# Optimization experiments

Hardware: AMD Instinct MI355X
Metric: run time of the kernel (lower is better)

## Reference

```python
import jax, jax.numpy as jnp
import numpy as np

B, TQ, TS, E, D = 8, 100, 100, 512, 512

def setup_inputs() -> dict:
    key = jax.random.key(0)
    k1, k2, k3, k4, k5 = jax.random.split(key, 5)
    src_reps = jax.random.normal(k1, (B, TQ, TS, E), dtype=jnp.float32)
    tgt_reps = jax.random.normal(k2, (B, TQ, TS, E), dtype=jnp.float32)
    mask = jnp.ones((B, TQ, TS), dtype=jnp.float32)
    # attn_1: Linear(2E -> D) with bias; attn_2: Linear(D -> 1) no bias
    W1 = jax.random.normal(k3, (2 * E, D), dtype=jnp.float32) / np.sqrt(2 * E)
    b1 = jax.random.normal(k4, (D,), dtype=jnp.float32) * 0.01
    w2 = jax.random.normal(k5, (D,), dtype=jnp.float32) / np.sqrt(D)
    return {"src_reps": src_reps, "tgt_reps": tgt_reps, "mask": mask,
            "W1": W1, "b1": b1, "w2": w2}

def reference(src_reps, tgt_reps, mask, W1, b1, w2):
    # cat over feature dim: [B,TQ,TS,2E]
    cat_reps = jnp.concatenate([src_reps, tgt_reps], axis=-1)
    # two small linears + tanh -> scores [B,TQ,TS]
    h = jnp.tanh(jnp.einsum('bqse,ed->bqsd', cat_reps, W1) + b1)
    attn_scores = jnp.einsum('bqsd,d->bqs', h, w2)
    attn_scores = mask * attn_scores  # multiplicative mask (as in source)
    attn_weights = jax.nn.softmax(attn_scores, axis=2)
    # weighted sum over src dim -> [B,TQ,E]
    attn_out = jnp.einsum('bqs,bqse->bqe', attn_weights, src_reps)
    return (attn_out, attn_weights)
```

## Files before the change

kernel.cpp:

```cpp
#include <hip/hip_runtime.h>
#include <hip/hip_bf16.h>

#define B_   8
#define TQ_  100
#define TS_  100
#define E_   512
#define D_   512
#define K_   1024
#define M_   (B_*TQ_*TS_)

#define BM   128
#define BK   64
#define NTHREADS 512

typedef __attribute__((ext_vector_type(4))) float f32x4;
typedef __attribute__((ext_vector_type(8))) short bf16x8;

__device__ __forceinline__ short f2bf(float f) {
  __hip_bfloat16 h = __float2bfloat16(f);
  return *reinterpret_cast<short*>(&h);
}

__device__ __forceinline__ float fast_tanh(float x) {
  float e = __expf(2.0f * x);
  return 1.0f - 2.0f / (e + 1.0f);
}

__device__ __forceinline__ void gld16(const void* g, void* l) {
  __builtin_amdgcn_global_load_lds(
      (const __attribute__((address_space(1))) unsigned int*)g,
      (__attribute__((address_space(3))) unsigned int*)l, 16, 0, 0);
}

__global__ void prep_w1(const float* __restrict__ W1, short* __restrict__ W1sw) {
  int idx = blockIdx.x * 256 + threadIdx.x;
  int k = idx >> 9;
  int n = idx & (D_ - 1);
  int byte = (k * 2) ^ ((n & 7) << 4);
  W1sw[(size_t)n * K_ + (byte >> 1)] = f2bf(W1[idx]);
}

__launch_bounds__(NTHREADS, 2)
__global__ void scores_kernel(const float* __restrict__ src,
                              const float* __restrict__ tgt,
                              const short* __restrict__ W1sw,
                              const float* __restrict__ b1,
                              const float* __restrict__ w2,
                              float* __restrict__ scores) {
  __shared__ __align__(16) char Alds[2][BM * 128];
  __shared__ __align__(16) char Blds[2][D_ * 128];

  const int tid  = threadIdx.x;
  const int wave = tid >> 6;
  const int lane = tid & 63;
  const int lr   = lane & 15;
  const int lg   = lane >> 4;
  const int wr   = wave >> 2;
  const int wc   = wave & 3;
  const int m0   = blockIdx.x * BM;

  f32x4 acc[4][8];
  #pragma unroll
  for (int i = 0; i < 4; i++)
    #pragma unroll
    for (int j = 0; j < 8; j++)
      acc[i][j] = (f32x4){0.f, 0.f, 0.f, 0.f};

  const int ra  = tid >> 2;
  const int kaf = (tid & 3) * 16;
  const int asw = (ra & 7) << 4;
  const size_t arow = (size_t)(m0 + ra) * E_;
  const size_t bgrow = (size_t)(tid >> 3) * 2048 + (size_t)(tid & 7) * 16;

  #define SBAR0       __builtin_amdgcn_sched_barrier(0)
  #define WAIT_LGKM0  { asm volatile("s_waitcnt lgkmcnt(0)" ::: "memory"); SBAR0; }

  #define ISSUE_A(K0)                                                          \
    { const float* Ap = (((K0) < E_) ? src : tgt) + arow + ((K0) & (E_-1)) + kaf; \
      r0 = *(const f32x4*)(Ap);                                                \
      r1 = *(const f32x4*)(Ap + 4);                                            \
      r2 = *(const f32x4*)(Ap + 8);                                            \
      r3 = *(const f32x4*)(Ap + 12); }

  #define ISSUE_B(K0, NX)                                                      \
    { _Pragma("unroll")                                                        \
      for (int j = 0; j < 8; j++)                                              \
        gld16((const char*)W1sw + (size_t)j * 131072 + (size_t)(K0) * 2 + bgrow, \
              Blds[NX] + j * 8192 + wave * 1024); }

  #define WRITE_A(NX)                                                          \
    { bf16x8 w0, w1;                                                           \
      w0[0]=f2bf(r0[0]); w0[1]=f2bf(r0[1]); w0[2]=f2bf(r0[2]); w0[3]=f2bf(r0[3]); \
      w0[4]=f2bf(r1[0]); w0[5]=f2bf(r1[1]); w0[6]=f2bf(r1[2]); w0[7]=f2bf(r1[3]); \
      w1[0]=f2bf(r2[0]); w1[1]=f2bf(r2[1]); w1[2]=f2bf(r2[2]); w1[3]=f2bf(r2[3]); \
      w1[4]=f2bf(r3[0]); w1[5]=f2bf(r3[1]); w1[6]=f2bf(r3[2]); w1[7]=f2bf(r3[3]); \
      int kb = kaf * 2;                                                        \
      *(bf16x8*)(Alds[NX] + ra * 128 + ( kb       ^ asw)) = w0;                \
      *(bf16x8*)(Alds[NX] + ra * 128 + ((kb + 16) ^ asw)) = w1; }

  #define HALF_K(KK, CUR)                                                      \
    { bf16x8 b[8];                                                             \
      _Pragma("unroll")                                                        \
      for (int ni = 0; ni < 8; ni++) {                                         \
        int n = wc * 128 + ni * 16 + lr;                                       \
        b[ni] = *(const bf16x8*)(Blds[CUR] + n * 128 +                         \
                    (((KK) * 64 + lg * 16) ^ ((n & 7) << 4)));                 \
      }                                                                        \
      WAIT_LGKM0;                                                              \
      __builtin_amdgcn_s_setprio(1);                                           \
      _Pragma("unroll")                                                        \
      for (int mi = 0; mi < 4; mi++)                                           \
        _Pragma("unroll")                                                      \
        for (int ni = 0; ni < 8; ni++)                                         \
          acc[mi][ni] = __builtin_amdgcn_mfma_f32_16x16x32_bf16(               \
              a[mi][KK], b[ni], acc[mi][ni], 0, 0, 0);                         \
      __builtin_amdgcn_s_setprio(0); }

  f32x4 r0, r1, r2, r3;

  ISSUE_A(0); SBAR0;
  ISSUE_B(0, 0); SBAR0;
  asm volatile("s_waitcnt vmcnt(8)" ::: "memory"); SBAR0;
  WRITE_A(0);
  asm volatile("s_waitcnt vmcnt(0) lgkmcnt(0)" ::: "memory"); SBAR0;
  __builtin_amdgcn_s_barrier();

  for (int t = 0; t < 16; ++t) {
    const int cur = t & 1;
    const int nxt = cur ^ 1;
    const bool pf = (t < 15);
    const int kn  = (t + 1) * BK;

    if (pf) {
      ISSUE_A(kn); SBAR0;
      ISSUE_B(kn, nxt); SBAR0;
    }

    bf16x8 a[4][2];
    #pragma unroll
    for (int mi = 0; mi < 4; mi++) {
      int row = wr * 64 + mi * 16 + lr;
      #pragma unroll
      for (int kk = 0; kk < 2; kk++)
        a[mi][kk] = *(const bf16x8*)(Alds[cur] + row * 128 +
                        ((kk * 64 + lg * 16) ^ ((row & 7) << 4)));
    }
    HALF_K(0, cur);
    HALF_K(1, cur);

    if (pf) {
      asm volatile("s_waitcnt vmcnt(8)" ::: "memory"); SBAR0;
      WRITE_A(nxt);
      asm volatile("s_waitcnt vmcnt(0) lgkmcnt(0)" ::: "memory"); SBAR0;
    }
    __builtin_amdgcn_s_barrier();
  }

  float* s_sc = (float*)Alds;
  if (tid < BM) s_sc[tid] = 0.0f;
  __syncthreads();

  float b1v[8], w2v[8];
  #pragma unroll
  for (int ni = 0; ni < 8; ni++) {
    int n = wc * 128 + ni * 16 + lr;
    b1v[ni] = b1[n];
    w2v[ni] = w2[n];
  }
  #pragma unroll
  for (int mi = 0; mi < 4; mi++) {
    #pragma unroll
    for (int r = 0; r < 4; r++) {
      float p = 0.0f;
      #pragma unroll
      for (int ni = 0; ni < 8; ni++)
        p += fast_tanh(acc[mi][ni][r] + b1v[ni]) * w2v[ni];
      p += __shfl_xor(p, 1);
      p += __shfl_xor(p, 2);
      p += __shfl_xor(p, 4);
      p += __shfl_xor(p, 8);
      if (lr == 0) atomicAdd(&s_sc[wr * 64 + mi * 16 + lg * 4 + r], p);
    }
  }
  __syncthreads();
  if (tid < BM) scores[m0 + tid] = s_sc[tid];
}

__global__ void softmax_wsum(const float* __restrict__ src,
                             const float* __restrict__ mask,
                             const float* __restrict__ scores,
                             float* __restrict__ out) {
  const int row = blockIdx.x;
  const int tid = threadIdx.x;
  __shared__ float s_e[TS_];

  float v = 0.0f;
  if (tid < TS_) {
    v = scores[row * TS_ + tid] * mask[row * TS_ + tid];
    s_e[tid] = v;
  }
  __syncthreads();
  float mx = -3.0e38f;
  for (int s = 0; s < TS_; s++) mx = fmaxf(mx, s_e[s]);
  __syncthreads();
  if (tid < TS_) s_e[tid] = __expf(v - mx);
  __syncthreads();
  float sum = 0.0f;
  for (int s = 0; s < TS_; s++) sum += s_e[s];
  const float inv = 1.0f / sum;

  float* out_attn = out;
  float* out_w    = out + (size_t)B_ * TQ_ * E_;
  if (tid < TS_) out_w[row * TS_ + tid] = s_e[tid] * inv;

  const float* sp = src + (size_t)row * TS_ * E_ + tid;
  float acc = 0.0f;
  #pragma unroll 4
  for (int s = 0; s < TS_; s++) acc = fmaf(s_e[s], sp[(size_t)s * E_], acc);
  out_attn[row * E_ + tid] = acc * inv;
}

extern "C" void kernel_launch(void* const* d_in, const int* in_sizes, int n_in,
                              void* d_out, int out_size, void* d_ws, size_t ws_size,
                              hipStream_t stream) {
  const float* src  = (const float*)d_in[0];
  const float* tgt  = (const float*)d_in[1];
  const float* mask = (const float*)d_in[2];
  const float* W1   = (const float*)d_in[3];
  const float* b1   = (const float*)d_in[4];
  const float* w2   = (const float*)d_in[5];

  short* W1sw   = (short*)d_ws;
  float* scores = (float*)((char*)d_ws + (size_t)D_ * K_ * 2);

  float* out = (float*)d_out;

  hipLaunchKernelGGL(prep_w1, dim3((K_ * D_) / 256), dim3(256), 0, stream, W1, W1sw);
  hipLaunchKernelGGL(scores_kernel, dim3(M_ / BM), dim3(NTHREADS), 0, stream,
                     src, tgt, W1sw, b1, w2, scores);
  hipLaunchKernelGGL(softmax_wsum, dim3(B_ * TQ_), dim3(512), 0, stream,
                     src, mask, scores, out);
}
```

Before: 190.8 us.

## Interleave global prefetch with quarter-tile MFMA phases in GEMM main loop

Splits each K-tile iteration into four phases, each reading a slice of A/B fragments from LDS and issuing 16 MFMAs. The global prefetches for the next B tile (in 8 chunks) and the next A tile are spread across those phases instead of being issued in one burst at the top of the iteration. The aim is to overlap memory traffic with matrix work more evenly and to lower register pressure by holding fewer fragments at once. In exchange it adds many more workgroup barriers per iteration and relies on hand-placed vmcnt waits, which must match the exact number of outstanding loads to stay correct.

```diff
diff --git a/kernel.cpp b/kernel.cpp
--- a/kernel.cpp
+++ b/kernel.cpp
@@ -70,90 +70,118 @@
   const int kaf = (tid & 3) * 16;
   const int asw = (ra & 7) << 4;
   const size_t arow = (size_t)(m0 + ra) * E_;
-  const size_t bgrow = (size_t)(tid >> 3) * 2048 + (size_t)(tid & 7) * 16;
 
   #define SBAR0       __builtin_amdgcn_sched_barrier(0)
   #define WAIT_LGKM0  { asm volatile("s_waitcnt lgkmcnt(0)" ::: "memory"); SBAR0; }
-
-  #define ISSUE_A(K0)                                                          \
-    { const float* Ap = (((K0) < E_) ? src : tgt) + arow + ((K0) & (E_-1)) + kaf; \
+  #define BARRIER     { __builtin_amdgcn_s_barrier(); SBAR0; }
+
+  #define ISSUE_B(R, KN, BNX)                                                  \
+    { const int rb = wc * 128 + (R) * 16 + wr * 8;                             \
+      gld16((const char*)W1sw + (size_t)(rb + (lane >> 3)) * 2048              \
+                + (size_t)(KN) * 2 + (size_t)((lane & 7) * 16),                \
+            (BNX) + rb * 128); }
+
+  #define ISSUE_AF32(KN)                                                       \
+    { const float* Ap = (((KN) < E_) ? src : tgt) + arow + ((KN) & (E_-1)) + kaf; \
       r0 = *(const f32x4*)(Ap);                                                \
       r1 = *(const f32x4*)(Ap + 4);                                            \
       r2 = *(const f32x4*)(Ap + 8);                                            \
       r3 = *(const f32x4*)(Ap + 12); }
 
-  #define ISSUE_B(K0, NX)                                                      \
-    { _Pragma("unroll")                                                        \
-      for (int j = 0; j < 8; j++)                                              \
-        gld16((const char*)W1sw + (size_t)j * 131072 + (size_t)(K0) * 2 + bgrow, \
-              Blds[NX] + j * 8192 + wave * 1024); }
-
-  #define WRITE_A(NX)                                                          \
+  #define WRITE_A(BUF)                                                         \
     { bf16x8 w0, w1;                                                           \
       w0[0]=f2bf(r0[0]); w0[1]=f2bf(r0[1]); w0[2]=f2bf(r0[2]); w0[3]=f2bf(r0[3]); \
       w0[4]=f2bf(r1[0]); w0[5]=f2bf(r1[1]); w0[6]=f2bf(r1[2]); w0[7]=f2bf(r1[3]); \
       w1[0]=f2bf(r2[0]); w1[1]=f2bf(r2[1]); w1[2]=f2bf(r2[2]); w1[3]=f2bf(r2[3]); \
       w1[4]=f2bf(r3[0]); w1[5]=f2bf(r3[1]); w1[6]=f2bf(r3[2]); w1[7]=f2bf(r3[3]); \
       int kb = kaf * 2;                                                        \
-      *(bf16x8*)(Alds[NX] + ra * 128 + ( kb       ^ asw)) = w0;                \
-      *(bf16x8*)(Alds[NX] + ra * 128 + ((kb + 16) ^ asw)) = w1; }
-
-  #define HALF_K(KK, CUR)                                                      \
-    { bf16x8 b[8];                                                             \
-      _Pragma("unroll")                                                        \
-      for (int ni = 0; ni < 8; ni++) {                                         \
-        int n = wc * 128 + ni * 16 + lr;                                       \
-        b[ni] = *(const bf16x8*)(Blds[CUR] + n * 128 +                         \
+      *(bf16x8*)((BUF) + ra * 128 + ( kb       ^ asw)) = w0;                   \
+      *(bf16x8*)((BUF) + ra * 128 + ((kb + 16) ^ asw)) = w1; }
+
+  #define RD_A(KK)                                                             \
+    { _Pragma("unroll")                                                        \
+      for (int mi = 0; mi < 4; mi++) {                                         \
+        int row = wr * 64 + mi * 16 + lr;                                      \
+        a[mi] = *(const bf16x8*)(Acur + row * 128 +                            \
+                    (((KK) * 64 + lg * 16) ^ ((row & 7) << 4)));               \
+      } }
+
+  #define RD_B(KK, H)                                                          \
+    { _Pragma("unroll")                                                        \
+      for (int nn = 0; nn < 4; nn++) {                                         \
+        int n = wc * 128 + ((H) * 4 + nn) * 16 + lr;                           \
+        b[nn] = *(const bf16x8*)(Bcur + n * 128 +                              \
                     (((KK) * 64 + lg * 16) ^ ((n & 7) << 4)));                 \
-      }                                                                        \
-      WAIT_LGKM0;                                                              \
-      __builtin_amdgcn_s_setprio(1);                                           \
+      } }
+
+  #define MFMA16(H)                                                            \
+    { __builtin_amdgcn_s_setprio(1);                                           \
       _Pragma("unroll")                                                        \
       for (int mi = 0; mi < 4; mi++)                                           \
         _Pragma("unroll")                                                      \
-        for (int ni = 0; ni < 8; ni++)                                         \
-          acc[mi][ni] = __builtin_amdgcn_mfma_f32_16x16x32_bf16(               \
-              a[mi][KK], b[ni], acc[mi][ni], 0, 0, 0);                         \
+        for (int nn = 0; nn < 4; nn++)                                         \
+          acc[mi][(H) * 4 + nn] = __builtin_amdgcn_mfma_f32_16x16x32_bf16(     \
+              a[mi], b[nn], acc[mi][(H) * 4 + nn], 0, 0, 0);                   \
       __builtin_amdgcn_s_setprio(0); }
 
-  f32x4 r0, r1, r2, r3;
-
-  ISSUE_A(0); SBAR0;
-  ISSUE_B(0, 0); SBAR0;
-  asm volatile("s_waitcnt vmcnt(8)" ::: "memory"); SBAR0;
-  WRITE_A(0);
-  asm volatile("s_waitcnt vmcnt(0) lgkmcnt(0)" ::: "memory"); SBAR0;
-  __builtin_amdgcn_s_barrier();
+  {
+    f32x4 r0, r1, r2, r3;
+    #pragma unroll
+    for (int r = 0; r < 8; r++) ISSUE_B(r, 0, Blds[0]);
+    ISSUE_AF32(0);
+    asm volatile("s_waitcnt vmcnt(0)" ::: "memory"); SBAR0;
+    WRITE_A(Alds[0]);
+    WAIT_LGKM0;
+    BARRIER;
+  }
 
   for (int t = 0; t < 16; ++t) {
-    const int cur = t & 1;
-    const int nxt = cur ^ 1;
+    char* Acur = Alds[t & 1];
+    char* Anxt = Alds[(t + 1) & 1];
+    char* Bcur = Blds[t & 1];
+    char* Bnxt = Blds[(t + 1) & 1];
     const bool pf = (t < 15);
     const int kn  = (t + 1) * BK;
-
+    bf16x8 a[4], b[4];
+    f32x4 r0, r1, r2, r3;
+
+    RD_A(0);
+    RD_B(0, 0);
     if (pf) {
-      ISSUE_A(kn); SBAR0;
-      ISSUE_B(kn, nxt); SBAR0;
-    }
-
-    bf16x8 a[4][2];
-    #pragma unroll
-    for (int mi = 0; mi < 4; mi++) {
-      int row = wr * 64 + mi * 16 + lr;
-      #pragma unroll
-      for (int kk = 0; kk < 2; kk++)
-        a[mi][kk] = *(const bf16x8*)(Alds[cur] + row * 128 +
-                        ((kk * 64 + lg * 16) ^ ((row & 7) << 4)));
-    }
-    HALF_K(0, cur);
-    HALF_K(1, cur);
-
+      ISSUE_B(0, kn, Bnxt); ISSUE_B(1, kn, Bnxt);
+      asm volatile("s_waitcnt vmcnt(2)" ::: "memory"); SBAR0;
+    } else {
+      asm volatile("s_waitcnt vmcnt(0)" ::: "memory"); SBAR0;
+    }
+    BARRIER; WAIT_LGKM0;
+    MFMA16(0);
+    BARRIER;
+
+    RD_B(0, 1);
     if (pf) {
-      asm volatile("s_waitcnt vmcnt(8)" ::: "memory"); SBAR0;
-      WRITE_A(nxt);
-      asm volatile("s_waitcnt vmcnt(0) lgkmcnt(0)" ::: "memory"); SBAR0;
-    }
-    __builtin_amdgcn_s_barrier();
+      ISSUE_B(2, kn, Bnxt); ISSUE_B(3, kn, Bnxt);
+      ISSUE_AF32(kn);
+    }
+    BARRIER; WAIT_LGKM0;
+    MFMA16(1);
+    BARRIER;
+
+    RD_A(1);
+    RD_B(1, 0);
+    if (pf) { ISSUE_B(4, kn, Bnxt); ISSUE_B(5, kn, Bnxt); }
+    BARRIER; WAIT_LGKM0;
+    MFMA16(0 + 2 - 2);
+    BARRIER;
+
+    RD_B(1, 1);
+    if (pf) {
+      ISSUE_B(6, kn, Bnxt); ISSUE_B(7, kn, Bnxt);
+      asm volatile("s_waitcnt vmcnt(4)" ::: "memory"); SBAR0;
+      WRITE_A(Anxt);
+    }
+    BARRIER; WAIT_LGKM0;
+    MFMA16(1);
+    BARRIER;
   }
 
   float* s_sc = (float*)Alds;
```

After: 190.8 us. No clear change (+0.0%).
